# Kernel tuning notes

Measured on AMD Instinct MI355X. Metric: run time of the kernel, lower is better.

## Reference

```python
import jax, jax.numpy as jnp
import numpy as np

TEMP = 0.5  # init kwarg `tmp`
NUM_CLASSES = 100


def setup_inputs() -> dict:
    key = jax.random.key(0)
    k1, k2 = jax.random.split(key)
    embedding = jax.random.normal(k1, (8192, 256), dtype=jnp.float32)
    label = jax.random.randint(k2, (8192,), 0, NUM_CLASSES, dtype=jnp.int64)
    return {"embedding": embedding, "label": label}


def reference(embedding, label):
    # Row-normalize -> pairwise cosine similarity [N, N]
    normed = embedding / jnp.linalg.norm(embedding, axis=1, keepdims=True)
    sim = (normed @ normed.T) / TEMP  # already divided by temperature

    N = embedding.shape[0]
    eye = jnp.eye(N, dtype=bool)

    # Denominator: sum of exp(sim) over off-diagonal entries per row
    exp_sim = jnp.exp(sim)
    row_sum = jnp.sum(jnp.where(eye, 0.0, exp_sim), axis=1)  # [N]

    # log(exp(sim_ij) / row_sum_i) = sim_ij - log(row_sum_i)
    log_prob = sim - jnp.log(row_sum)[:, None]

    # Positive mask: same label, i != j
    pos_mask = (label[:, None] == label[None, :]) & ~eye
    n_i = jnp.sum(pos_mask, axis=1)  # positives per anchor

    inner = jnp.sum(jnp.where(pos_mask, log_prob, 0.0), axis=1)  # [N]
    per_anchor = jnp.where(n_i > 0, -inner / jnp.maximum(n_i, 1).astype(sim.dtype), 0.0)
    return jnp.sum(per_anchor)
```

## Files before the change

kernel.cpp:

```cpp
#include <hip/hip_runtime.h>
#include <hip/hip_bf16.h>
#include <stdint.h>

#define N    8192
#define D    256
#define NCLS 100

static constexpr float TEMP    = 0.5f;
static constexpr float SCALE_F = 1.69864360f;
static constexpr float LN2     = 0.69314718055994531f;

#define NSLOT 130

typedef float f32x4 __attribute__((ext_vector_type(4)));
typedef long  lx2  __attribute__((ext_vector_type(2)));

__device__ __forceinline__ unsigned short f2bf(float f) {
  union { float f; unsigned int u; } x; x.f = f;
  unsigned int r = x.u + 0x7fffu + ((x.u >> 16) & 1u);
  return (unsigned short)(r >> 16);
}
__device__ __forceinline__ float bf2f(unsigned short b) {
  union { unsigned int u; float f; } x; x.u = ((unsigned int)b) << 16;
  return x.f;
}


__global__ __launch_bounds__(256) void normalize_kernel(
    const float* __restrict__ emb, const long long* __restrict__ label,
    unsigned short* __restrict__ abf, unsigned char* __restrict__ a8,
    int* __restrict__ cnt, int* __restrict__ list) {
  const int row  = blockIdx.x * 4 + (threadIdx.x >> 6);
  const int lane = threadIdx.x & 63;
  const float4 v = ((const float4*)(emb + (size_t)row * D))[lane];
  float ss = v.x * v.x + v.y * v.y + v.z * v.z + v.w * v.w;
#pragma unroll
  for (int off = 1; off < 64; off <<= 1) ss += __shfl_xor(ss, off);
  const float s = rsqrtf(ss) * SCALE_F;
  const float x = v.x * s, y = v.y * s, z = v.z * s, wv = v.w * s;

  ushort4 o;
  o.x = f2bf(x); o.y = f2bf(y); o.z = f2bf(z); o.w = f2bf(wv);
  ((ushort4*)(abf + (size_t)row * D))[lane] = o;

  int p = __builtin_amdgcn_cvt_pk_fp8_f32(x, y, 0, false);
  p = __builtin_amdgcn_cvt_pk_fp8_f32(z, wv, p, true);
  *(int*)(a8 + (size_t)(row >> 4) * 4096 + (lane >> 4) * 1024 +
          ((lane >> 1) & 3) * 256 + (row & 15) * 16 + ((lane >> 3) & 1) * 8 +
          (lane & 1) * 4) = p;

  if (lane == 0) {
    const int c = (int)label[row];
    const int slot = atomicAdd(cnt + c, 1);
    list[c * 256 + slot] = row;
  }
}

struct TileCoord { int x, y; };
__device__ __forceinline__ TileCoord tri_decode(int b) {
  int x = (int)((-1.0f + sqrtf(1.0f + 8.0f * (float)b)) * 0.5f);
  while ((x + 1) * (x + 2) / 2 <= b) ++x;
  while (x * (x + 1) / 2 > b) --x;
  return {x, b - x * (x + 1) / 2};
}

__global__ __launch_bounds__(256, 2) void simexp_rowsum_kernel(
    const unsigned char* __restrict__ A, float* __restrict__ part) {
  const int tid  = threadIdx.x;
  const int w    = tid >> 6;
  const int lane = tid & 63;
  const int quad = lane >> 4;
  const int l15  = lane & 15;

  const TileCoord tc = tri_decode(blockIdx.x);
  const int x = tc.x, y = tc.y;
  const int row0 = y << 7;
  const int col0 = x << 7;
  const bool diag = (x == y);
  const int wm  = (w & 1) * 64;
  const int jn0 = (w >> 1) * 64;

  if (diag && wm > jn0) {
    part[((size_t)y * NSLOT + 2 * x) * 128 + 64 + lane] = 0.f;
    part[((size_t)x * NSLOT + 129) * 128 + lane] = 0.f;
    return;
  }
  const bool needmask = diag && (wm == jn0);

  const unsigned char* Ap = A + (size_t)((row0 >> 4) + (w & 1) * 4) * 4096;
  const unsigned char* Bp = A + (size_t)((col0 >> 4) + (w >> 1) * 4) * 4096;
  const int lo = quad * 256 + l15 * 16;

  lx2 aF[4][4], bF[4][4];
  f32x4 acc[4][4];
#pragma unroll
  for (int mt = 0; mt < 4; ++mt)
#pragma unroll
    for (int nt = 0; nt < 4; ++nt) acc[mt][nt] = (f32x4){0.f, 0.f, 0.f, 0.f};

#pragma unroll
  for (int mt = 0; mt < 4; ++mt)
    aF[mt][0] = *(const lx2*)(Ap + mt * 4096 + lo);
#pragma unroll
  for (int nt = 0; nt < 4; ++nt)
    bF[nt][0] = *(const lx2*)(Bp + nt * 4096 + lo);

#pragma unroll
  for (int kq = 0; kq < 4; ++kq) {
    if (kq < 3) {
#pragma unroll
      for (int mt = 0; mt < 4; ++mt)
        aF[mt][kq + 1] = *(const lx2*)(Ap + mt * 4096 + (kq + 1) * 1024 + lo);
#pragma unroll
      for (int nt = 0; nt < 4; ++nt)
        bF[nt][kq + 1] = *(const lx2*)(Bp + nt * 4096 + (kq + 1) * 1024 + lo);
    }
#pragma unroll
    for (int kkl = 0; kkl < 2; ++kkl)
#pragma unroll
      for (int mt = 0; mt < 4; ++mt)
#pragma unroll
        for (int nt = 0; nt < 4; ++nt)
          acc[mt][nt] = __builtin_amdgcn_mfma_f32_16x16x32_fp8_fp8(
              aF[mt][kq][kkl], bF[nt][kq][kkl], acc[mt][nt], 0, 0, 0);
  }

  float rowpart[4][4];
  float colpart[4] = {0.f, 0.f, 0.f, 0.f};
#pragma unroll
  for (int mt = 0; mt < 4; ++mt)
#pragma unroll
    for (int e = 0; e < 4; ++e) rowpart[mt][e] = 0.f;
#pragma unroll
  for (int mt = 0; mt < 4; ++mt)
#pragma unroll
    for (int nt = 0; nt < 4; ++nt)
#pragma unroll
      for (int e = 0; e < 4; ++e) {
        float v = __builtin_amdgcn_exp2f(acc[mt][nt][e]);
        if (needmask) {
          const int iw = mt * 16 + quad * 4 + e;
          const int jw = nt * 16 + l15;
          v = (iw < jw) ? v : 0.f;
        }
        rowpart[mt][e] += v;
        colpart[nt] += v;
      }

  const int rslot = 2 * x + (jn0 >> 6);
  const int cslot = diag ? (128 + (wm >> 6)) : (2 * y + (wm >> 6));
  float* rowdst = part + ((size_t)y * NSLOT + rslot) * 128 + wm;
  float* coldst = part + ((size_t)x * NSLOT + cslot) * 128 + jn0;

#pragma unroll
  for (int nt = 0; nt < 4; ++nt) {
    float v = colpart[nt];
    v += __shfl_xor(v, 16);
    v += __shfl_xor(v, 32);
    if (quad == 0) coldst[nt * 16 + l15] = v;
  }
#pragma unroll
  for (int mt = 0; mt < 4; ++mt)
#pragma unroll
    for (int e = 0; e < 4; ++e) {
      float v = rowpart[mt][e];
      v += __shfl_xor(v, 1);
      v += __shfl_xor(v, 2);
      v += __shfl_xor(v, 4);
      v += __shfl_xor(v, 8);
      if (l15 == 0) rowdst[mt * 16 + quad * 4 + e] = v;
    }
}

__global__ __launch_bounds__(256) void finalize_kernel(
    const unsigned short* __restrict__ abf, const float* __restrict__ part,
    const long long* __restrict__ label, const int* __restrict__ cnt,
    const int* __restrict__ list, float* __restrict__ out) {
  __shared__ float red[4];
  __shared__ int rows_l[256];
  const int tid  = threadIdx.x;
  const int w    = tid >> 6;
  const int lane = tid & 63;

  if (blockIdx.x < NCLS) {
    const int c = blockIdx.x;
    const int m = cnt[c];
    if (m <= 1) return;
    if (tid < m) rows_l[tid] = list[c * 256 + tid];
    __syncthreads();
    float acc = 0.f;
    for (int s = 0; s < m; ++s)
      acc += bf2f(abf[(size_t)rows_l[s] * D + tid]);
    float v = acc * acc;
#pragma unroll
    for (int off = 1; off < 64; off <<= 1) v += __shfl_xor(v, off);
    if (lane == 0) red[w] = v;
    __syncthreads();
    if (tid == 0) {
      const float ssq = red[0] + red[1] + red[2] + red[3];
      const float term = (ssq * LN2 - 2.0f * (float)m) / (float)(m - 1);
      atomicAdd(out, -term);
    }
  } else {
    const int i = (blockIdx.x - NCLS) * 256 + tid;
    const int band = i >> 7, r = i & 127;
    const float* ps = part + (size_t)band * NSLOT * 128 + r;
    float rs = 0.f;
#pragma unroll 13
    for (int s = 0; s < NSLOT; ++s) rs += ps[(size_t)s * 128];
    const int c = (int)label[i];
    float v = 0.f;
    if (cnt[c] > 1)
      v = __builtin_amdgcn_logf(rs) * LN2;
#pragma unroll
    for (int off = 1; off < 64; off <<= 1) v += __shfl_xor(v, off);
    if (lane == 0) red[w] = v;
    __syncthreads();
    if (tid == 0)
      atomicAdd(out, red[0] + red[1] + red[2] + red[3]);
  }
}

extern "C" void kernel_launch(void* const* d_in, const int* in_sizes, int n_in,
                              void* d_out, int out_size, void* d_ws,
                              size_t ws_size, hipStream_t stream) {
  const float* emb = (const float*)d_in[0];
  const long long* label = (const long long*)d_in[1];
  float* out = (float*)d_out;

  char* ws = (char*)d_ws;
  unsigned short* abf = (unsigned short*)ws;
  unsigned char* a8 = (unsigned char*)(ws + (size_t)N * D * 2);
  float* part = (float*)(ws + (size_t)N * D * 3);
  int* cnt = (int*)(ws + (size_t)N * D * 3 + (size_t)64 * NSLOT * 128 * 4);
  int* list = cnt + 128;

  hipMemsetAsync(cnt, 0, 128 * 4, stream);
  hipMemsetAsync(out, 0, sizeof(float), stream);

  normalize_kernel<<<N / 4, 256, 0, stream>>>(emb, label, abf, a8, cnt, list);

  simexp_rowsum_kernel<<<2080, 256, 0, stream>>>(a8, part);

  finalize_kernel<<<NCLS + N / 256, 256, 0, stream>>>(abf, part, label, cnt,
                                                      list, out);
}
```

Measured before the change: 122.8 us.

## Stage tiles in LDS via global_load_lds with 8 waves per block

The similarity kernel now stages both 128x256 fp8 operand tiles into shared memory with direct global-to-LDS loads. It runs 512 threads per block, so each of 8 waves computes a 64x32 sub-tile read from LDS instead of each wave loading its own operands from global memory. The partial-sum slot layout grows to 384 slots, and it is now zeroed inside the normalize kernel so that waves which skip masked diagonal work leave valid zeros behind. This cuts redundant global and L2 traffic and raises the wave count per block. In exchange it needs 64KB of LDS per block, which may limit occupancy, and it adds a barrier plus a larger reduction in finalize.

```diff
diff --git a/kernel.cpp b/kernel.cpp
--- a/kernel.cpp
+++ b/kernel.cpp
@@ -10,7 +10,7 @@
 static constexpr float SCALE_F = 1.69864360f;
 static constexpr float LN2     = 0.69314718055994531f;
 
-#define NSLOT 130
+#define NSLOT 384
 
 typedef float f32x4 __attribute__((ext_vector_type(4)));
 typedef long  lx2  __attribute__((ext_vector_type(2)));
@@ -24,12 +24,17 @@
   union { unsigned int u; float f; } x; x.u = ((unsigned int)b) << 16;
   return x.f;
 }
+__device__ __forceinline__ void gld16(const void* g, void* l) {
+  __builtin_amdgcn_global_load_lds(
+      (const __attribute__((address_space(1))) unsigned int*)g,
+      (__attribute__((address_space(3))) unsigned int*)l, 16, 0, 0);
+}
 
 
 __global__ __launch_bounds__(256) void normalize_kernel(
     const float* __restrict__ emb, const long long* __restrict__ label,
     unsigned short* __restrict__ abf, unsigned char* __restrict__ a8,
-    int* __restrict__ cnt, int* __restrict__ list) {
+    float* __restrict__ part, int* __restrict__ cnt, int* __restrict__ list) {
   const int row  = blockIdx.x * 4 + (threadIdx.x >> 6);
   const int lane = threadIdx.x & 63;
   const float4 v = ((const float4*)(emb + (size_t)row * D))[lane];
@@ -48,6 +53,10 @@
   *(int*)(a8 + (size_t)(row >> 4) * 4096 + (lane >> 4) * 1024 +
           ((lane >> 1) & 3) * 256 + (row & 15) * 16 + ((lane >> 3) & 1) * 8 +
           (lane & 1) * 4) = p;
+
+  const int gtid = blockIdx.x * 256 + threadIdx.x;
+#pragma unroll
+  for (int k = 0; k < 6; ++k) part[(size_t)k * 524288 + gtid] = 0.f;
 
   if (lane == 0) {
     const int c = (int)label[row];
@@ -64,8 +73,10 @@
   return {x, b - x * (x + 1) / 2};
 }
 
-__global__ __launch_bounds__(256, 2) void simexp_rowsum_kernel(
+__global__ __launch_bounds__(512, 4) void simexp_rowsum_kernel(
     const unsigned char* __restrict__ A, float* __restrict__ part) {
+  __shared__ __align__(16) unsigned char sa[128 * 256];
+  __shared__ __align__(16) unsigned char sb[128 * 256];
   const int tid  = threadIdx.x;
   const int w    = tid >> 6;
   const int lane = tid & 63;
@@ -78,55 +89,53 @@
   const int col0 = x << 7;
   const bool diag = (x == y);
   const int wm  = (w & 1) * 64;
-  const int jn0 = (w >> 1) * 64;
-
-  if (diag && wm > jn0) {
-    part[((size_t)y * NSLOT + 2 * x) * 128 + 64 + lane] = 0.f;
-    part[((size_t)x * NSLOT + 129) * 128 + lane] = 0.f;
-    return;
-  }
-  const bool needmask = diag && (wm == jn0);
-
-  const unsigned char* Ap = A + (size_t)((row0 >> 4) + (w & 1) * 4) * 4096;
-  const unsigned char* Bp = A + (size_t)((col0 >> 4) + (w >> 1) * 4) * 4096;
-  const int lo = quad * 256 + l15 * 16;
-
-  lx2 aF[4][4], bF[4][4];
-  f32x4 acc[4][4];
-#pragma unroll
-  for (int mt = 0; mt < 4; ++mt)
-#pragma unroll
-    for (int nt = 0; nt < 4; ++nt) acc[mt][nt] = (f32x4){0.f, 0.f, 0.f, 0.f};
-
-#pragma unroll
-  for (int mt = 0; mt < 4; ++mt)
-    aF[mt][0] = *(const lx2*)(Ap + mt * 4096 + lo);
-#pragma unroll
-  for (int nt = 0; nt < 4; ++nt)
-    bF[nt][0] = *(const lx2*)(Bp + nt * 4096 + lo);
+  const int jqi = w >> 1;
+  const int jq  = jqi * 32;
+
+#pragma unroll
+  for (int p = 0; p < 4; ++p) {
+    const int seg = w * 4 + p;
+    gld16(A + (size_t)(row0 >> 4) * 4096 + seg * 1024 + lane * 16,
+          sa + seg * 1024);
+    gld16(A + (size_t)(col0 >> 4) * 4096 + seg * 1024 + lane * 16,
+          sb + seg * 1024);
+  }
+  __syncthreads();
+
+  if (diag && jq + 32 <= wm) return;
+  const bool needmask = diag && (jq < wm + 64);
+
+  const int pam = (w & 1) * 4;
+  const int pbn = jqi * 2;
+  const int lo  = quad * 256 + l15 * 16;
+
+  f32x4 acc[4][2];
+#pragma unroll
+  for (int mt = 0; mt < 4; ++mt)
+#pragma unroll
+    for (int nt = 0; nt < 2; ++nt) acc[mt][nt] = (f32x4){0.f, 0.f, 0.f, 0.f};
 
 #pragma unroll
   for (int kq = 0; kq < 4; ++kq) {
-    if (kq < 3) {
+    lx2 aF[4], bF[2];
+#pragma unroll
+    for (int mt = 0; mt < 4; ++mt)
+      aF[mt] = *(const lx2*)(sa + (pam + mt) * 4096 + kq * 1024 + lo);
+#pragma unroll
+    for (int nt = 0; nt < 2; ++nt)
+      bF[nt] = *(const lx2*)(sb + (pbn + nt) * 4096 + kq * 1024 + lo);
+#pragma unroll
+    for (int kkl = 0; kkl < 2; ++kkl)
 #pragma unroll
       for (int mt = 0; mt < 4; ++mt)
-        aF[mt][kq + 1] = *(const lx2*)(Ap + mt * 4096 + (kq + 1) * 1024 + lo);
-#pragma unroll
-      for (int nt = 0; nt < 4; ++nt)
-        bF[nt][kq + 1] = *(const lx2*)(Bp + nt * 4096 + (kq + 1) * 1024 + lo);
-    }
-#pragma unroll
-    for (int kkl = 0; kkl < 2; ++kkl)
-#pragma unroll
-      for (int mt = 0; mt < 4; ++mt)
-#pragma unroll
-        for (int nt = 0; nt < 4; ++nt)
+#pragma unroll
+        for (int nt = 0; nt < 2; ++nt)
           acc[mt][nt] = __builtin_amdgcn_mfma_f32_16x16x32_fp8_fp8(
-              aF[mt][kq][kkl], bF[nt][kq][kkl], acc[mt][nt], 0, 0, 0);
+              aF[mt][kkl], bF[nt][kkl], acc[mt][nt], 0, 0, 0);
   }
 
   float rowpart[4][4];
-  float colpart[4] = {0.f, 0.f, 0.f, 0.f};
+  float colpart[2] = {0.f, 0.f};
 #pragma unroll
   for (int mt = 0; mt < 4; ++mt)
 #pragma unroll
@@ -134,26 +143,24 @@
 #pragma unroll
   for (int mt = 0; mt < 4; ++mt)
 #pragma unroll
-    for (int nt = 0; nt < 4; ++nt)
+    for (int nt = 0; nt < 2; ++nt)
 #pragma unroll
       for (int e = 0; e < 4; ++e) {
         float v = __builtin_amdgcn_exp2f(acc[mt][nt][e]);
         if (needmask) {
-          const int iw = mt * 16 + quad * 4 + e;
-          const int jw = nt * 16 + l15;
+          const int iw = wm + mt * 16 + quad * 4 + e;
+          const int jw = jq + nt * 16 + l15;
           v = (iw < jw) ? v : 0.f;
         }
         rowpart[mt][e] += v;
         colpart[nt] += v;
       }
 
-  const int rslot = 2 * x + (jn0 >> 6);
-  const int cslot = diag ? (128 + (wm >> 6)) : (2 * y + (wm >> 6));
-  float* rowdst = part + ((size_t)y * NSLOT + rslot) * 128 + wm;
-  float* coldst = part + ((size_t)x * NSLOT + cslot) * 128 + jn0;
-
-#pragma unroll
-  for (int nt = 0; nt < 4; ++nt) {
+  float* rowdst = part + ((size_t)y * NSLOT + 4 * x + jqi) * 128 + wm;
+  float* coldst = part + ((size_t)x * NSLOT + 256 + 2 * y + (w & 1)) * 128 + jq;
+
+#pragma unroll
+  for (int nt = 0; nt < 2; ++nt) {
     float v = colpart[nt];
     v += __shfl_xor(v, 16);
     v += __shfl_xor(v, 32);
@@ -206,7 +213,7 @@
     const int band = i >> 7, r = i & 127;
     const float* ps = part + (size_t)band * NSLOT * 128 + r;
     float rs = 0.f;
-#pragma unroll 13
+#pragma unroll 16
     for (int s = 0; s < NSLOT; ++s) rs += ps[(size_t)s * 128];
     const int c = (int)label[i];
     float v = 0.f;
@@ -238,9 +245,10 @@
   hipMemsetAsync(cnt, 0, 128 * 4, stream);
   hipMemsetAsync(out, 0, sizeof(float), stream);
 
-  normalize_kernel<<<N / 4, 256, 0, stream>>>(emb, label, abf, a8, cnt, list);
-
-  simexp_rowsum_kernel<<<2080, 256, 0, stream>>>(a8, part);
+  normalize_kernel<<<N / 4, 256, 0, stream>>>(emb, label, abf, a8, part, cnt,
+                                              list);
+
+  simexp_rowsum_kernel<<<2080, 512, 0, stream>>>(a8, part);
 
   finalize_kernel<<<NCLS + N / 256, 256, 0, stream>>>(abf, part, label, cnt,
                                                       list, out);
```

New measurement: 130.3 us. +6.1%, slower.

## Use 256x256 tiles with LDS staging via global_load_lds in simexp kernel

Applied to the files above, without the earlier changes.

The similarity/exp kernel moves from 128x128 tiles with 4 waves loading fragments directly from global memory to 256x256 tiles with 16 waves. The A and B panels are staged in shared memory through async global-to-LDS loads, split into two K halves so the second half's load overlaps compute on the first. This raises operand reuse and cuts the block count from 2080 to 528. Partial-sum slots double to match the wider tiles, and the lower-diagonal slots are now zeroed in the normalize kernel rather than written by skipped waves. The costs are 128KB of LDS per block, which limits occupancy, and fewer blocks to spread across CUs.

```diff
diff --git a/kernel.cpp b/kernel.cpp
--- a/kernel.cpp
+++ b/kernel.cpp
@@ -10,7 +10,7 @@
 static constexpr float SCALE_F = 1.69864360f;
 static constexpr float LN2     = 0.69314718055994531f;
 
-#define NSLOT 130
+#define NSLOT 260
 
 typedef float f32x4 __attribute__((ext_vector_type(4)));
 typedef long  lx2  __attribute__((ext_vector_type(2)));
@@ -24,12 +24,17 @@
   union { unsigned int u; float f; } x; x.u = ((unsigned int)b) << 16;
   return x.f;
 }
+__device__ __forceinline__ void gld16(const void* g, void* l) {
+  __builtin_amdgcn_global_load_lds(
+      (const __attribute__((address_space(1))) unsigned int*)g,
+      (__attribute__((address_space(3))) unsigned int*)l, 16, 0, 0);
+}
 
 
 __global__ __launch_bounds__(256) void normalize_kernel(
     const float* __restrict__ emb, const long long* __restrict__ label,
     unsigned short* __restrict__ abf, unsigned char* __restrict__ a8,
-    int* __restrict__ cnt, int* __restrict__ list) {
+    float* __restrict__ part, int* __restrict__ cnt, int* __restrict__ list) {
   const int row  = blockIdx.x * 4 + (threadIdx.x >> 6);
   const int lane = threadIdx.x & 63;
   const float4 v = ((const float4*)(emb + (size_t)row * D))[lane];
@@ -48,6 +53,13 @@
   *(int*)(a8 + (size_t)(row >> 4) * 4096 + (lane >> 4) * 1024 +
           ((lane >> 1) & 3) * 256 + (row & 15) * 16 + ((lane >> 3) & 1) * 8 +
           (lane & 1) * 4) = p;
+
+  const int gtid = blockIdx.x * 256 + threadIdx.x;
+#pragma unroll
+  for (int k = 0; k < 5; ++k) {
+    const size_t idx = (size_t)k * 524288 + gtid;
+    if (idx < (size_t)32 * NSLOT * 256) part[idx] = 0.f;
+  }
 
   if (lane == 0) {
     const int c = (int)label[row];
@@ -64,34 +76,55 @@
   return {x, b - x * (x + 1) / 2};
 }
 
-__global__ __launch_bounds__(256, 2) void simexp_rowsum_kernel(
+__global__ __launch_bounds__(1024, 4) void simexp_rowsum_kernel(
     const unsigned char* __restrict__ A, float* __restrict__ part) {
+  __shared__ __align__(16) unsigned char sa[16 * 4096];
+  __shared__ __align__(16) unsigned char sb[16 * 4096];
   const int tid  = threadIdx.x;
   const int w    = tid >> 6;
   const int lane = tid & 63;
   const int quad = lane >> 4;
   const int l15  = lane & 15;
+  const int wr   = w & 3;
+  const int wc   = w >> 2;
 
   const TileCoord tc = tri_decode(blockIdx.x);
   const int x = tc.x, y = tc.y;
-  const int row0 = y << 7;
-  const int col0 = x << 7;
+  const int pr0 = y << 4;
+  const int pc0 = x << 4;
   const bool diag = (x == y);
-  const int wm  = (w & 1) * 64;
-  const int jn0 = (w >> 1) * 64;
-
-  if (diag && wm > jn0) {
-    part[((size_t)y * NSLOT + 2 * x) * 128 + 64 + lane] = 0.f;
-    part[((size_t)x * NSLOT + 129) * 128 + lane] = 0.f;
-    return;
-  }
-  const bool needmask = diag && (wm == jn0);
-
-  const unsigned char* Ap = A + (size_t)((row0 >> 4) + (w & 1) * 4) * 4096;
-  const unsigned char* Bp = A + (size_t)((col0 >> 4) + (w >> 1) * 4) * 4096;
-  const int lo = quad * 256 + l15 * 16;
-
-  lx2 aF[4][4], bF[4][4];
+  const bool needmask  = diag && (wc == wr);
+  const bool skipstore = diag && (wc < wr);
+
+  const int rot = blockIdx.x & 31;
+
+#pragma unroll
+  for (int p = 0; p < 2; ++p) {
+    const int s = (w * 2 + p + rot) & 31;
+    gld16(A + (size_t)(pr0 + (s >> 1)) * 4096 + (s & 1) * 1024 + lane * 16,
+          sa + (s >> 1) * 4096 + (s & 1) * 1024);
+    const int t = (w * 2 + p + rot + 16) & 31;
+    gld16(A + (size_t)(pc0 + (t >> 1)) * 4096 + (t & 1) * 1024 + lane * 16,
+          sb + (t >> 1) * 4096 + (t & 1) * 1024);
+  }
+  __syncthreads();
+
+#pragma unroll
+  for (int p = 0; p < 2; ++p) {
+    const int s = (w * 2 + p + rot) & 31;
+    gld16(A + (size_t)(pr0 + (s >> 1)) * 4096 + 2048 + (s & 1) * 1024 +
+              lane * 16,
+          sa + (s >> 1) * 4096 + 2048 + (s & 1) * 1024);
+    const int t = (w * 2 + p + rot + 16) & 31;
+    gld16(A + (size_t)(pc0 + (t >> 1)) * 4096 + 2048 + (t & 1) * 1024 +
+              lane * 16,
+          sb + (t >> 1) * 4096 + 2048 + (t & 1) * 1024);
+  }
+
+  const int pam = wr * 4;
+  const int pbn = wc * 4;
+  const int lo  = quad * 256 + l15 * 16;
+
   f32x4 acc[4][4];
 #pragma unroll
   for (int mt = 0; mt < 4; ++mt)
@@ -99,22 +132,14 @@
     for (int nt = 0; nt < 4; ++nt) acc[mt][nt] = (f32x4){0.f, 0.f, 0.f, 0.f};
 
 #pragma unroll
-  for (int mt = 0; mt < 4; ++mt)
-    aF[mt][0] = *(const lx2*)(Ap + mt * 4096 + lo);
-#pragma unroll
-  for (int nt = 0; nt < 4; ++nt)
-    bF[nt][0] = *(const lx2*)(Bp + nt * 4096 + lo);
-
-#pragma unroll
-  for (int kq = 0; kq < 4; ++kq) {
-    if (kq < 3) {
-#pragma unroll
-      for (int mt = 0; mt < 4; ++mt)
-        aF[mt][kq + 1] = *(const lx2*)(Ap + mt * 4096 + (kq + 1) * 1024 + lo);
-#pragma unroll
-      for (int nt = 0; nt < 4; ++nt)
-        bF[nt][kq + 1] = *(const lx2*)(Bp + nt * 4096 + (kq + 1) * 1024 + lo);
-    }
+  for (int kq = 0; kq < 2; ++kq) {
+    lx2 aF[4], bF[4];
+#pragma unroll
+    for (int mt = 0; mt < 4; ++mt)
+      aF[mt] = *(const lx2*)(sa + (pam + mt) * 4096 + kq * 1024 + lo);
+#pragma unroll
+    for (int nt = 0; nt < 4; ++nt)
+      bF[nt] = *(const lx2*)(sb + (pbn + nt) * 4096 + kq * 1024 + lo);
 #pragma unroll
     for (int kkl = 0; kkl < 2; ++kkl)
 #pragma unroll
@@ -122,7 +147,27 @@
 #pragma unroll
         for (int nt = 0; nt < 4; ++nt)
           acc[mt][nt] = __builtin_amdgcn_mfma_f32_16x16x32_fp8_fp8(
-              aF[mt][kq][kkl], bF[nt][kq][kkl], acc[mt][nt], 0, 0, 0);
+              aF[mt][kkl], bF[nt][kkl], acc[mt][nt], 0, 0, 0);
+  }
+  __syncthreads();
+
+#pragma unroll
+  for (int kq = 2; kq < 4; ++kq) {
+    lx2 aF[4], bF[4];
+#pragma unroll
+    for (int mt = 0; mt < 4; ++mt)
+      aF[mt] = *(const lx2*)(sa + (pam + mt) * 4096 + kq * 1024 + lo);
+#pragma unroll
+    for (int nt = 0; nt < 4; ++nt)
+      bF[nt] = *(const lx2*)(sb + (pbn + nt) * 4096 + kq * 1024 + lo);
+#pragma unroll
+    for (int kkl = 0; kkl < 2; ++kkl)
+#pragma unroll
+      for (int mt = 0; mt < 4; ++mt)
+#pragma unroll
+        for (int nt = 0; nt < 4; ++nt)
+          acc[mt][nt] = __builtin_amdgcn_mfma_f32_16x16x32_fp8_fp8(
+              aF[mt][kkl], bF[nt][kkl], acc[mt][nt], 0, 0, 0);
   }
 
   float rowpart[4][4];
@@ -147,29 +192,32 @@
         colpart[nt] += v;
       }
 
-  const int rslot = 2 * x + (jn0 >> 6);
-  const int cslot = diag ? (128 + (wm >> 6)) : (2 * y + (wm >> 6));
-  float* rowdst = part + ((size_t)y * NSLOT + rslot) * 128 + wm;
-  float* coldst = part + ((size_t)x * NSLOT + cslot) * 128 + jn0;
-
-#pragma unroll
-  for (int nt = 0; nt < 4; ++nt) {
-    float v = colpart[nt];
-    v += __shfl_xor(v, 16);
-    v += __shfl_xor(v, 32);
-    if (quad == 0) coldst[nt * 16 + l15] = v;
-  }
-#pragma unroll
-  for (int mt = 0; mt < 4; ++mt)
-#pragma unroll
-    for (int e = 0; e < 4; ++e) {
-      float v = rowpart[mt][e];
-      v += __shfl_xor(v, 1);
-      v += __shfl_xor(v, 2);
-      v += __shfl_xor(v, 4);
-      v += __shfl_xor(v, 8);
-      if (l15 == 0) rowdst[mt * 16 + quad * 4 + e] = v;
+  if (!skipstore) {
+    float* rowdst =
+        part + ((size_t)y * NSLOT + 4 * x + wc) * 256 + wr * 64;
+    float* coldst =
+        part + ((size_t)x * NSLOT + (diag ? (256 + wr) : (128 + 4 * y + wr))) *
+                   256 + wc * 64;
+
+#pragma unroll
+    for (int nt = 0; nt < 4; ++nt) {
+      float v = colpart[nt];
+      v += __shfl_xor(v, 16);
+      v += __shfl_xor(v, 32);
+      if (quad == 0) coldst[nt * 16 + l15] = v;
     }
+#pragma unroll
+    for (int mt = 0; mt < 4; ++mt)
+#pragma unroll
+      for (int e = 0; e < 4; ++e) {
+        float v = rowpart[mt][e];
+        v += __shfl_xor(v, 1);
+        v += __shfl_xor(v, 2);
+        v += __shfl_xor(v, 4);
+        v += __shfl_xor(v, 8);
+        if (l15 == 0) rowdst[mt * 16 + quad * 4 + e] = v;
+      }
+  }
 }
 
 __global__ __launch_bounds__(256) void finalize_kernel(
@@ -203,11 +251,11 @@
     }
   } else {
     const int i = (blockIdx.x - NCLS) * 256 + tid;
-    const int band = i >> 7, r = i & 127;
-    const float* ps = part + (size_t)band * NSLOT * 128 + r;
+    const int band = i >> 8, r = i & 255;
+    const float* ps = part + (size_t)band * NSLOT * 256 + r;
     float rs = 0.f;
 #pragma unroll 13
-    for (int s = 0; s < NSLOT; ++s) rs += ps[(size_t)s * 128];
+    for (int s = 0; s < NSLOT; ++s) rs += ps[(size_t)s * 256];
     const int c = (int)label[i];
     float v = 0.f;
     if (cnt[c] > 1)
@@ -232,15 +280,16 @@
   unsigned short* abf = (unsigned short*)ws;
   unsigned char* a8 = (unsigned char*)(ws + (size_t)N * D * 2);
   float* part = (float*)(ws + (size_t)N * D * 3);
-  int* cnt = (int*)(ws + (size_t)N * D * 3 + (size_t)64 * NSLOT * 128 * 4);
+  int* cnt = (int*)(ws + (size_t)N * D * 3 + (size_t)32 * NSLOT * 256 * 4);
   int* list = cnt + 128;
 
   hipMemsetAsync(cnt, 0, 128 * 4, stream);
   hipMemsetAsync(out, 0, sizeof(float), stream);
 
-  normalize_kernel<<<N / 4, 256, 0, stream>>>(emb, label, abf, a8, cnt, list);
-
-  simexp_rowsum_kernel<<<2080, 256, 0, stream>>>(a8, part);
+  normalize_kernel<<<N / 4, 256, 0, stream>>>(emb, label, abf, a8, part, cnt,
+                                              list);
+
+  simexp_rowsum_kernel<<<528, 1024, 0, stream>>>(a8, part);
 
   finalize_kernel<<<NCLS + N / 256, 256, 0, stream>>>(abf, part, label, cnt,
                                                       list, out);
```

Result: slower. 132.0 us (+7.5%).
